# Kernel tuning notes

Hardware: AMD Instinct MI355X
Metric: run time of the kernel (lower is better)

Reference implementation:

```python
import jax, jax.numpy as jnp
import numpy as np

B, N, S, K, R = 4, 8192, 2048, 64, 0.2  # batch, points, centroids, neighbors, ball radius
EPS = 1e-5  # BatchNorm eps


def fps_indices(x, n_samples):
    """Farthest point sampling; returns int32 [B, n_samples] indices."""
    xs = jax.lax.stop_gradient(x)
    Bb, Nn, _ = xs.shape

    def step(carry, _):
        dist, farthest = carry
        centroid = jnp.take_along_axis(xs, farthest[:, None, None], axis=1)  # [B,1,3]
        d = jnp.sum((xs - centroid) ** 2, axis=-1)  # [B,N]
        dist = jnp.minimum(dist, d)
        nxt = jnp.argmax(dist, axis=-1).astype(jnp.int32)
        return (dist, nxt), farthest

    init = (jnp.full((Bb, Nn), 1e10, xs.dtype), jnp.zeros((Bb,), jnp.int32))
    _, idxs = jax.lax.scan(step, init, None, length=n_samples)  # [S,B]
    return jnp.transpose(idxs)  # [B,S]


def ball_query(x, centroids, radius, k):
    """First k point indices within radius of each centroid, -1 padded. int32 [B,S,k]."""
    xs = jax.lax.stop_gradient(x)
    cs = jax.lax.stop_gradient(centroids)
    Nn = xs.shape[1]
    d2 = jnp.sum((cs[:, :, None, :] - xs[:, None, :, :]) ** 2, axis=-1)  # [B,S,N]
    cand = jnp.where(d2 < radius * radius, jnp.arange(Nn, dtype=jnp.int32), Nn)
    neg_topk, _ = jax.lax.top_k(-cand, k)  # k smallest candidate indices
    idx = -neg_topk
    return jnp.where(idx == Nn, -1, idx)


def _forward(x, x_complete, layers, idx_fps, idx_ball):
    centroids = jnp.take_along_axis(x, idx_fps[..., None], axis=1)  # [B,S,3]
    valid = idx_ball >= 0  # [B,S,K]
    sidx = jnp.maximum(idx_ball, 0)
    gather = lambda pts: jax.vmap(lambda p, i: p[i])(pts, sidx)  # [B,S,K,C]
    x_local = gather(x) - centroids[:, :, None, :]  # relative coords
    feats = jnp.concatenate([gather(x_complete), x_local], axis=-1)  # [B,S,K,67]
    h = feats.reshape(B, S * K, -1).transpose(0, 2, 1)  # [B,67,S*K]
    for (W, b, g, bt, m, v) in layers:  # Conv1d(k=1) -> BN(eval) -> ReLU
        h = jnp.einsum('oc,bcn->bon', W, h) + b[None, :, None]
        h = (h - m[None, :, None]) * (g * jax.lax.rsqrt(v + EPS))[None, :, None] + bt[None, :, None]
        h = jax.nn.relu(h)
    h = h.reshape(B, -1, S, K)  # [B,128,S,K]
    h = jnp.where(valid[:, None, :, :], h, -jnp.inf)  # mask invalid neighbors
    pooled = jnp.max(h, axis=3)  # masked max pool over neighborhood
    return centroids, pooled.transpose(0, 2, 1)  # [B,S,3], [B,S,128]


def setup_inputs():
    key = jax.random.key(0)
    ks = jax.random.split(key, 8)
    x = jax.random.uniform(ks[0], (B, N, 3), jnp.float32)
    x_complete = jax.random.normal(ks[1], (B, N, 64), jnp.float32)
    dims = [67, 64, 64, 128]
    inp = {'x': x, 'x_complete': x_complete}
    for i in range(3):
        cin, cout = dims[i], dims[i + 1]
        kk = jax.random.split(ks[2 + i], 6)
        inp[f'W{i+1}'] = jax.random.normal(kk[0], (cout, cin), jnp.float32) * 0.05
        inp[f'b{i+1}'] = jax.random.normal(kk[1], (cout,), jnp.float32) * 0.02
        inp[f'g{i+1}'] = 1.0 + 0.1 * jax.random.normal(kk[2], (cout,), jnp.float32)
        inp[f'bt{i+1}'] = jax.random.normal(kk[3], (cout,), jnp.float32) * 0.02
        inp[f'm{i+1}'] = jax.random.normal(kk[4], (cout,), jnp.float32) * 0.05
        inp[f'v{i+1}'] = jax.random.uniform(kk[5], (cout,), jnp.float32, minval=0.5, maxval=1.5)
    return inp


def reference(x, x_complete, W1, b1, g1, bt1, m1, v1, W2, b2, g2, bt2, m2, v2, W3, b3, g3, bt3, m3, v3):
    idx_fps = fps_indices(x, S)
    cen_sg = jnp.take_along_axis(jax.lax.stop_gradient(x), idx_fps[..., None], axis=1)
    idx_ball = ball_query(x, cen_sg, R, K)
    layers = ((W1, b1, g1, bt1, m1, v1), (W2, b2, g2, bt2, m2, v2), (W3, b3, g3, bt3, m3, v3))
    return _forward(x, x_complete, layers, idx_fps, idx_ball)
```

## Files before the change

kernel.cpp:

```cpp
#include <hip/hip_runtime.h>
#include <math.h>

#define BATCH 4
#define NPTS  8192
#define NSAMP 2048
#define KNBR  64
#define EPSF  1e-5f

typedef float v2f __attribute__((ext_vector_type(2)));

__global__ void prep_kernel(const float* __restrict__ W1, const float* __restrict__ W2,
                            const float* __restrict__ W3,
                            float* __restrict__ W1t, float* __restrict__ W2t,
                            float* __restrict__ W3t) {
    int t = threadIdx.x;
    for (int i = t; i < 64 * 67; i += 256) { int o = i / 67, c = i % 67; W1t[c * 64 + o] = W1[i]; }
    for (int i = t; i < 64 * 64; i += 256) { int o = i >> 6, c = i & 63; W2t[c * 64 + o] = W2[i]; }
    for (int i = t; i < 128 * 64; i += 256) { int o = i >> 6, c = i & 63; W3t[c * 128 + o] = W3[i]; }
}

#define DPP_FMAX(v, ctrl)                                                            \
    do {                                                                             \
        int _t = __builtin_amdgcn_update_dpp(0, __float_as_int(v), ctrl, 0xf, 0xf, true); \
        (v) = fmaxf((v), __int_as_float(_t));                                        \
    } while (0)

__global__ __launch_bounds__(512) void fps_kernel(const float* __restrict__ x,
                                                  float* __restrict__ cen_out) {
#pragma clang fp contract(off)
    const int b = blockIdx.x;
    const int tid = threadIdx.x;
    const int lane = tid & 63;
    const int wid = tid >> 6;
    __shared__ float sx[NPTS], sy[NPTS], sz[NPTS];
    __shared__ __align__(16) float pd[2][8];
    __shared__ int pi[2];
    __shared__ int hist[NSAMP];

    const float* xb = x + (size_t)b * NPTS * 3;
    for (int i = tid; i < NPTS; i += 512) {
        sx[i] = xb[3 * i + 0];
        sy[i] = xb[3 * i + 1];
        sz[i] = xb[3 * i + 2];
    }
    if (tid == 0) { pi[0] = 0x7fffffff; pi[1] = 0x7fffffff; }
    __syncthreads();

    v2f px[8], py[8], pz[8], dist[8];
#pragma unroll
    for (int j = 0; j < 8; j++) {
        int p = tid * 16 + 2 * j;
        px[j] = (v2f){sx[p], sx[p + 1]};
        py[j] = (v2f){sy[p], sy[p + 1]};
        pz[j] = (v2f){sz[p], sz[p + 1]};
        dist[j] = (v2f){1e10f, 1e10f};
    }

    int cur = 0;
    for (int s = 0; s < NSAMP; s++) {
        float cx = sx[cur], cy = sy[cur], cz = sz[cur];
        if (tid == 0) hist[s] = cur;
        const v2f cvx = (v2f){cx, cx}, cvy = (v2f){cy, cy}, cvz = (v2f){cz, cz};
        v2f m = (v2f){-1.0f, -1.0f};
#pragma unroll
        for (int j = 0; j < 8; j++) {
            v2f dx = px[j] - cvx;
            v2f dy = py[j] - cvy;
            v2f dz = pz[j] - cvz;
            v2f d = ((dx * dx) + (dy * dy)) + (dz * dz);
            v2f dm;
            dm.x = fminf(dist[j].x, d.x);
            dm.y = fminf(dist[j].y, d.y);
            dist[j] = dm;
            m.x = fmaxf(m.x, dm.x);
            m.y = fmaxf(m.y, dm.y);
        }
        float bestd = fmaxf(m.x, m.y);
        float w = bestd;
        DPP_FMAX(w, 0x111);
        DPP_FMAX(w, 0x112);
        DPP_FMAX(w, 0x114);
        DPP_FMAX(w, 0x118);
        DPP_FMAX(w, 0x142);
        DPP_FMAX(w, 0x143);
        const int p = s & 1;
        if (lane == 63) pd[p][wid] = w;
        __syncthreads();
        float4 da = *(const float4*)&pd[p][0];
        float4 db = *(const float4*)&pd[p][4];
        float bmax = fmaxf(fmaxf(fmaxf(da.x, da.y), fmaxf(da.z, da.w)),
                           fmaxf(fmaxf(db.x, db.y), fmaxf(db.z, db.w)));
        if (tid == 0) pi[1 - p] = 0x7fffffff;
        int local = 0x7fffffff;
#pragma unroll
        for (int j = 0; j < 8; j++) {
            if (dist[j].x == bmax) local = min(local, tid * 16 + 2 * j);
            if (dist[j].y == bmax) local = min(local, tid * 16 + 2 * j + 1);
        }
        if (local != 0x7fffffff) atomicMin(&pi[p], local);
        __syncthreads();
        cur = pi[p];
    }

    __syncthreads();
    for (int i = tid; i < NSAMP; i += 512) {
        int idx = hist[i];
        float* o = cen_out + ((size_t)b * NSAMP + i) * 3;
        o[0] = sx[idx]; o[1] = sy[idx]; o[2] = sz[idx];
    }
}

__global__ __launch_bounds__(256) void ball_kernel(const float* __restrict__ x,
                                                   const float* __restrict__ cen,
                                                   int* __restrict__ idxb) {
    const int wid = threadIdx.x >> 6, lane = threadIdx.x & 63;
    const int id = blockIdx.x * 4 + wid;
    const int b = id >> 11;
    const float r2 = (float)(0.2 * 0.2);
    const float cx = cen[3 * id], cy = cen[3 * id + 1], cz = cen[3 * id + 2];
    const float* xb = x + (size_t)b * NPTS * 3;

    int count = 0;
    for (int base = 0; base < NPTS && count < KNBR; base += 64) {
        int p = base + lane;
        float pxv = xb[3 * p], pyv = xb[3 * p + 1], pzv = xb[3 * p + 2];
        float dx = __fsub_rn(cx, pxv);
        float dy = __fsub_rn(cy, pyv);
        float dz = __fsub_rn(cz, pzv);
        float d2 = __fadd_rn(__fadd_rn(__fmul_rn(dx, dx), __fmul_rn(dy, dy)), __fmul_rn(dz, dz));
        bool hit = d2 < r2;
        unsigned long long m = __ballot(hit);
        if (hit) {
            int pos = count + __popcll(m & ((1ull << lane) - 1ull));
            if (pos < KNBR) idxb[(size_t)id * KNBR + pos] = p;
        }
        count += (int)__popcll(m);
    }
    for (int pos = count + lane; pos < KNBR; pos += 64)
        idxb[(size_t)id * KNBR + pos] = -1;
}

__global__ __launch_bounds__(256) void mlp_kernel(
    const float* __restrict__ x, const float* __restrict__ xc,
    const float* __restrict__ cen, const int* __restrict__ idxb,
    const float* __restrict__ W1t, const float* __restrict__ b1, const float* __restrict__ g1,
    const float* __restrict__ bt1, const float* __restrict__ m1, const float* __restrict__ v1,
    const float* __restrict__ W2t, const float* __restrict__ b2, const float* __restrict__ g2,
    const float* __restrict__ bt2, const float* __restrict__ m2, const float* __restrict__ v2,
    const float* __restrict__ W3t, const float* __restrict__ b3, const float* __restrict__ g3,
    const float* __restrict__ bt3, const float* __restrict__ m3, const float* __restrict__ v3,
    float* __restrict__ pooled) {
    const int wid = threadIdx.x >> 6, lane = threadIdx.x & 63;
    const int id = blockIdx.x * 4 + wid;
    const int b = id >> 11;
    __shared__ float sred[4][64][33];

    int il = idxb[(size_t)id * KNBR + lane];
    bool valid = il >= 0;
    int ik = valid ? il : 0;

    float cx = cen[3 * id], cy = cen[3 * id + 1], cz = cen[3 * id + 2];
    const float* xp = x + ((size_t)b * NPTS + ik) * 3;
    const float* xcp = xc + ((size_t)b * NPTS + ik) * 64;

    float h1[64];
#pragma unroll
    for (int o = 0; o < 64; o++) h1[o] = 0.f;
#pragma unroll
    for (int c4 = 0; c4 < 16; c4++) {
        float4 t = ((const float4*)xcp)[c4];
        float tv0 = t.x, tv1 = t.y, tv2 = t.z, tv3 = t.w;
#pragma unroll
        for (int o = 0; o < 64; o++) h1[o] = fmaf(W1t[(c4 * 4 + 0) * 64 + o], tv0, h1[o]);
#pragma unroll
        for (int o = 0; o < 64; o++) h1[o] = fmaf(W1t[(c4 * 4 + 1) * 64 + o], tv1, h1[o]);
#pragma unroll
        for (int o = 0; o < 64; o++) h1[o] = fmaf(W1t[(c4 * 4 + 2) * 64 + o], tv2, h1[o]);
#pragma unroll
        for (int o = 0; o < 64; o++) h1[o] = fmaf(W1t[(c4 * 4 + 3) * 64 + o], tv3, h1[o]);
    }
    {
        float xl0 = xp[0] - cx, xl1 = xp[1] - cy, xl2 = xp[2] - cz;
#pragma unroll
        for (int o = 0; o < 64; o++) h1[o] = fmaf(W1t[64 * 64 + o], xl0, h1[o]);
#pragma unroll
        for (int o = 0; o < 64; o++) h1[o] = fmaf(W1t[65 * 64 + o], xl1, h1[o]);
#pragma unroll
        for (int o = 0; o < 64; o++) h1[o] = fmaf(W1t[66 * 64 + o], xl2, h1[o]);
    }
#pragma unroll
    for (int o = 0; o < 64; o++) {
        float sc = g1[o] * rsqrtf(v1[o] + EPSF);
        h1[o] = fmaxf(fmaf(h1[o] + b1[o] - m1[o], sc, bt1[o]), 0.f);
    }

    float h2[64];
#pragma unroll
    for (int o = 0; o < 64; o++) h2[o] = 0.f;
#pragma unroll
    for (int c = 0; c < 64; c++) {
        float hv = h1[c];
#pragma unroll
        for (int o = 0; o < 64; o++) h2[o] = fmaf(W2t[c * 64 + o], hv, h2[o]);
    }
#pragma unroll
    for (int o = 0; o < 64; o++) {
        float sc = g2[o] * rsqrtf(v2[o] + EPSF);
        h2[o] = fmaxf(fmaf(h2[o] + b2[o] - m2[o], sc, bt2[o]), 0.f);
    }

    for (int ch = 0; ch < 4; ch++) {
        float acc[32];
#pragma unroll
        for (int oo = 0; oo < 32; oo++) acc[oo] = 0.f;
#pragma unroll
        for (int c = 0; c < 64; c++) {
            float hv = h2[c];
#pragma unroll
            for (int oo = 0; oo < 32; oo++)
                acc[oo] = fmaf(W3t[c * 128 + ch * 32 + oo], hv, acc[oo]);
        }
#pragma unroll
        for (int oo = 0; oo < 32; oo++) {
            int o = ch * 32 + oo;
            float sc = g3[o] * rsqrtf(v3[o] + EPSF);
            float t = fmaxf(fmaf(acc[oo] + b3[o] - m3[o], sc, bt3[o]), 0.f);
            sred[wid][lane][oo] = valid ? t : -INFINITY;
        }
        __syncthreads();
        {
            int c = lane & 31, half = lane >> 5;
            float mx = -INFINITY;
#pragma unroll
            for (int r = 0; r < 32; r++) mx = fmaxf(mx, sred[wid][half * 32 + r][c]);
            mx = fmaxf(mx, __shfl_xor(mx, 32, 64));
            if (lane < 32) pooled[(size_t)id * 128 + ch * 32 + c] = mx;
        }
        __syncthreads();
    }
}

extern "C" void kernel_launch(void* const* d_in, const int* in_sizes, int n_in,
                              void* d_out, int out_size, void* d_ws, size_t ws_size,
                              hipStream_t stream) {
    const float* x  = (const float*)d_in[0];
    const float* xc = (const float*)d_in[1];
    const float* W1 = (const float*)d_in[2];
    const float* b1 = (const float*)d_in[3];
    const float* g1 = (const float*)d_in[4];
    const float* bt1 = (const float*)d_in[5];
    const float* m1 = (const float*)d_in[6];
    const float* v1 = (const float*)d_in[7];
    const float* W2 = (const float*)d_in[8];
    const float* b2 = (const float*)d_in[9];
    const float* g2 = (const float*)d_in[10];
    const float* bt2 = (const float*)d_in[11];
    const float* m2 = (const float*)d_in[12];
    const float* v2 = (const float*)d_in[13];
    const float* W3 = (const float*)d_in[14];
    const float* b3 = (const float*)d_in[15];
    const float* g3 = (const float*)d_in[16];
    const float* bt3 = (const float*)d_in[17];
    const float* m3 = (const float*)d_in[18];
    const float* v3 = (const float*)d_in[19];

    float* out = (float*)d_out;
    float* cen = out;
    float* pooled = out + (size_t)BATCH * NSAMP * 3;

    int* idxb = (int*)d_ws;
    float* W1t = (float*)((char*)d_ws + (size_t)BATCH * NSAMP * KNBR * 4);
    float* W2t = W1t + 67 * 64;
    float* W3t = W2t + 64 * 64;

    prep_kernel<<<1, 256, 0, stream>>>(W1, W2, W3, W1t, W2t, W3t);
    fps_kernel<<<BATCH, 512, 0, stream>>>(x, cen);
    ball_kernel<<<(BATCH * NSAMP) / 4, 256, 0, stream>>>(x, cen, idxb);
    mlp_kernel<<<(BATCH * NSAMP) / 4, 256, 0, stream>>>(
        x, xc, cen, idxb,
        W1t, b1, g1, bt1, m1, v1,
        W2t, b2, g2, bt2, m2, v2,
        W3t, b3, g3, bt3, m3, v3,
        pooled);
}
```

Measured before the change: 2.418 ms.

## Restructure FPS argmax to one barrier per step with in-wave index selection

The farthest-point-sampling kernel now uses 256 threads, each holding 32 points instead of 16, and builds the per-thread max with a tree reduction. After the DPP max, each wave finds its own argmax through a ballot and readlane. It writes the (value, index) pair to shared memory, so each iteration needs one barrier instead of two plus an atomicMin. This targets the serial per-step synchronisation cost in the 2048-step loop, at the price of more registers per thread and fewer waves to hide latency. Ties across waves still resolve to the lowest index, because the wave comparison uses strict greater-than in wave order.

New measurement: 2.295 ms. -5.1%, faster.

```diff
diff --git a/kernel.cpp b/kernel.cpp
--- a/kernel.cpp
+++ b/kernel.cpp
@@ -25,45 +25,44 @@
         (v) = fmaxf((v), __int_as_float(_t));                                        \
     } while (0)
 
-__global__ __launch_bounds__(512) void fps_kernel(const float* __restrict__ x,
-                                                  float* __restrict__ cen_out) {
+__global__ __launch_bounds__(256, 1) void fps_kernel(const float* __restrict__ x,
+                                                     float* __restrict__ cen_out) {
 #pragma clang fp contract(off)
     const int b = blockIdx.x;
     const int tid = threadIdx.x;
     const int lane = tid & 63;
     const int wid = tid >> 6;
     __shared__ float sx[NPTS], sy[NPTS], sz[NPTS];
-    __shared__ __align__(16) float pd[2][8];
-    __shared__ int pi[2];
+    __shared__ __align__(16) float sd[2][4];
+    __shared__ __align__(16) int   si[2][4];
     __shared__ int hist[NSAMP];
 
     const float* xb = x + (size_t)b * NPTS * 3;
-    for (int i = tid; i < NPTS; i += 512) {
+    for (int i = tid; i < NPTS; i += 256) {
         sx[i] = xb[3 * i + 0];
         sy[i] = xb[3 * i + 1];
         sz[i] = xb[3 * i + 2];
     }
-    if (tid == 0) { pi[0] = 0x7fffffff; pi[1] = 0x7fffffff; }
     __syncthreads();
 
-    v2f px[8], py[8], pz[8], dist[8];
-#pragma unroll
-    for (int j = 0; j < 8; j++) {
-        int p = tid * 16 + 2 * j;
-        px[j] = (v2f){sx[p], sx[p + 1]};
-        py[j] = (v2f){sy[p], sy[p + 1]};
-        pz[j] = (v2f){sz[p], sz[p + 1]};
+    v2f px[16], py[16], pz[16], dist[16];
+    const int base = tid * 32;
+#pragma unroll
+    for (int j = 0; j < 16; j++) {
+        int p = base + 2 * j;
+        px[j] = *(const v2f*)&sx[p];
+        py[j] = *(const v2f*)&sy[p];
+        pz[j] = *(const v2f*)&sz[p];
         dist[j] = (v2f){1e10f, 1e10f};
     }
 
     int cur = 0;
+    float cx = sx[0], cy = sy[0], cz = sz[0];
     for (int s = 0; s < NSAMP; s++) {
-        float cx = sx[cur], cy = sy[cur], cz = sz[cur];
         if (tid == 0) hist[s] = cur;
         const v2f cvx = (v2f){cx, cx}, cvy = (v2f){cy, cy}, cvz = (v2f){cz, cz};
-        v2f m = (v2f){-1.0f, -1.0f};
-#pragma unroll
-        for (int j = 0; j < 8; j++) {
+#pragma unroll
+        for (int j = 0; j < 16; j++) {
             v2f dx = px[j] - cvx;
             v2f dy = py[j] - cvy;
             v2f dz = pz[j] - cvz;
@@ -72,10 +71,18 @@
             dm.x = fminf(dist[j].x, d.x);
             dm.y = fminf(dist[j].y, d.y);
             dist[j] = dm;
-            m.x = fmaxf(m.x, dm.x);
-            m.y = fmaxf(m.y, dm.y);
-        }
-        float bestd = fmaxf(m.x, m.y);
+        }
+        float t[16];
+#pragma unroll
+        for (int j = 0; j < 16; j++) t[j] = fmaxf(dist[j].x, dist[j].y);
+#pragma unroll
+        for (int off = 8; off >= 1; off >>= 1) {
+#pragma unroll
+            for (int j = 0; j < 8; j++)
+                if (j < off) t[j] = fmaxf(t[j], t[j + off]);
+        }
+        float bestd = t[0];
+
         float w = bestd;
         DPP_FMAX(w, 0x111);
         DPP_FMAX(w, 0x112);
@@ -83,27 +90,35 @@
         DPP_FMAX(w, 0x118);
         DPP_FMAX(w, 0x142);
         DPP_FMAX(w, 0x143);
+        const float wmax = __int_as_float(__builtin_amdgcn_readlane(__float_as_int(w), 63));
+
+        unsigned long long mask = __ballot(bestd == wmax);
+        int wl = (int)__builtin_ctzll(mask);
+
+        int lj = 0;
+#pragma unroll
+        for (int j = 15; j >= 0; j--) {
+            if (dist[j].y == wmax) lj = 2 * j + 1;
+            if (dist[j].x == wmax) lj = 2 * j;
+        }
+        int widx = __builtin_amdgcn_readlane(base + lj, wl);
+
         const int p = s & 1;
-        if (lane == 63) pd[p][wid] = w;
+        if (lane == 0) { sd[p][wid] = wmax; si[p][wid] = widx; }
         __syncthreads();
-        float4 da = *(const float4*)&pd[p][0];
-        float4 db = *(const float4*)&pd[p][4];
-        float bmax = fmaxf(fmaxf(fmaxf(da.x, da.y), fmaxf(da.z, da.w)),
-                           fmaxf(fmaxf(db.x, db.y), fmaxf(db.z, db.w)));
-        if (tid == 0) pi[1 - p] = 0x7fffffff;
-        int local = 0x7fffffff;
-#pragma unroll
-        for (int j = 0; j < 8; j++) {
-            if (dist[j].x == bmax) local = min(local, tid * 16 + 2 * j);
-            if (dist[j].y == bmax) local = min(local, tid * 16 + 2 * j + 1);
-        }
-        if (local != 0x7fffffff) atomicMin(&pi[p], local);
-        __syncthreads();
-        cur = pi[p];
+
+        float4 dv = *(const float4*)&sd[p][0];
+        int4   iv = *(const int4*)&si[p][0];
+        float bb = dv.x; int bi = iv.x;
+        if (dv.y > bb) { bb = dv.y; bi = iv.y; }
+        if (dv.z > bb) { bb = dv.z; bi = iv.z; }
+        if (dv.w > bb) { bb = dv.w; bi = iv.w; }
+        cur = bi;
+        cx = sx[cur]; cy = sy[cur]; cz = sz[cur];
     }
 
     __syncthreads();
-    for (int i = tid; i < NSAMP; i += 512) {
+    for (int i = tid; i < NSAMP; i += 256) {
         int idx = hist[i];
         float* o = cen_out + ((size_t)b * NSAMP + i) * 3;
         o[0] = sx[idx]; o[1] = sy[idx]; o[2] = sz[idx];
@@ -274,7 +289,7 @@
     float* W3t = W2t + 64 * 64;
 
     prep_kernel<<<1, 256, 0, stream>>>(W1, W2, W3, W1t, W2t, W3t);
-    fps_kernel<<<BATCH, 512, 0, stream>>>(x, cen);
+    fps_kernel<<<BATCH, 256, 0, stream>>>(x, cen);
     ball_kernel<<<(BATCH * NSAMP) / 4, 256, 0, stream>>>(x, cen, idxb);
     mlp_kernel<<<(BATCH * NSAMP) / 4, 256, 0, stream>>>(
         x, xc, cen, idxb,
```

## Resolve FPS argmax per wave with ballot/readlane, dropping second barrier and atomics

Applied to the files above, without the earlier changes.

Each FPS step now finds the per-wave max and its lowest index in registers using DPP, readlane and ballot. Every wave writes a (value, index) pair to shared memory, and all threads reduce the 8 pairs after a single barrier. This removes the second __syncthreads and the shared atomicMin from every one of the 2048 serial iterations. Points are stored as float4 in LDS so the next centroid comes from one vector load, which adds LDS footprint. Ties across waves go to the lower wave index, and within a wave the first lane wins, which keeps the lowest-index argmax semantics.

Result: faster. 2.345 ms (-3.0%).

```diff
diff --git a/kernel.cpp b/kernel.cpp
--- a/kernel.cpp
+++ b/kernel.cpp
@@ -25,43 +25,42 @@
         (v) = fmaxf((v), __int_as_float(_t));                                        \
     } while (0)
 
-__global__ __launch_bounds__(512) void fps_kernel(const float* __restrict__ x,
-                                                  float* __restrict__ cen_out) {
+__global__ __launch_bounds__(512, 1) void fps_kernel(const float* __restrict__ x,
+                                                     float* __restrict__ cen_out) {
 #pragma clang fp contract(off)
     const int b = blockIdx.x;
     const int tid = threadIdx.x;
     const int lane = tid & 63;
     const int wid = tid >> 6;
-    __shared__ float sx[NPTS], sy[NPTS], sz[NPTS];
-    __shared__ __align__(16) float pd[2][8];
-    __shared__ int pi[2];
+    __shared__ float4 sp[NPTS];
+    __shared__ __align__(32) float sd[2][8];
+    __shared__ __align__(32) int   si[2][8];
     __shared__ int hist[NSAMP];
 
     const float* xb = x + (size_t)b * NPTS * 3;
     for (int i = tid; i < NPTS; i += 512) {
-        sx[i] = xb[3 * i + 0];
-        sy[i] = xb[3 * i + 1];
-        sz[i] = xb[3 * i + 2];
-    }
-    if (tid == 0) { pi[0] = 0x7fffffff; pi[1] = 0x7fffffff; }
+        sp[i] = (float4){xb[3 * i + 0], xb[3 * i + 1], xb[3 * i + 2], 0.f};
+    }
     __syncthreads();
 
     v2f px[8], py[8], pz[8], dist[8];
+    const int base = tid * 16;
 #pragma unroll
     for (int j = 0; j < 8; j++) {
-        int p = tid * 16 + 2 * j;
-        px[j] = (v2f){sx[p], sx[p + 1]};
-        py[j] = (v2f){sy[p], sy[p + 1]};
-        pz[j] = (v2f){sz[p], sz[p + 1]};
+        float4 a = sp[base + 2 * j];
+        float4 c = sp[base + 2 * j + 1];
+        px[j] = (v2f){a.x, c.x};
+        py[j] = (v2f){a.y, c.y};
+        pz[j] = (v2f){a.z, c.z};
         dist[j] = (v2f){1e10f, 1e10f};
     }
 
     int cur = 0;
+    float4 cp = sp[0];
     for (int s = 0; s < NSAMP; s++) {
-        float cx = sx[cur], cy = sy[cur], cz = sz[cur];
         if (tid == 0) hist[s] = cur;
-        const v2f cvx = (v2f){cx, cx}, cvy = (v2f){cy, cy}, cvz = (v2f){cz, cz};
-        v2f m = (v2f){-1.0f, -1.0f};
+        const v2f cvx = (v2f){cp.x, cp.x}, cvy = (v2f){cp.y, cp.y}, cvz = (v2f){cp.z, cp.z};
+        float t[8];
 #pragma unroll
         for (int j = 0; j < 8; j++) {
             v2f dx = px[j] - cvx;
@@ -72,10 +71,12 @@
             dm.x = fminf(dist[j].x, d.x);
             dm.y = fminf(dist[j].y, d.y);
             dist[j] = dm;
-            m.x = fmaxf(m.x, dm.x);
-            m.y = fmaxf(m.y, dm.y);
-        }
-        float bestd = fmaxf(m.x, m.y);
+            t[j] = fmaxf(dm.x, dm.y);
+        }
+        float m01 = fmaxf(t[0], t[1]), m23 = fmaxf(t[2], t[3]);
+        float m45 = fmaxf(t[4], t[5]), m67 = fmaxf(t[6], t[7]);
+        float bestd = fmaxf(fmaxf(m01, m23), fmaxf(m45, m67));
+
         float w = bestd;
         DPP_FMAX(w, 0x111);
         DPP_FMAX(w, 0x112);
@@ -83,30 +84,53 @@
         DPP_FMAX(w, 0x118);
         DPP_FMAX(w, 0x142);
         DPP_FMAX(w, 0x143);
+        const float wmax = __int_as_float(__builtin_amdgcn_readlane(__float_as_int(w), 63));
+
+        unsigned long long mask = __ballot(bestd == wmax);
+        int wl = (int)__builtin_ctzll(mask);
+
+        int c[8];
+#pragma unroll
+        for (int j = 0; j < 8; j++) {
+            int cc = 0x7fffffff;
+            cc = (dist[j].y == wmax) ? (2 * j + 1) : cc;
+            cc = (dist[j].x == wmax) ? (2 * j) : cc;
+            c[j] = cc;
+        }
+        int n01 = min(c[0], c[1]), n23 = min(c[2], c[3]);
+        int n45 = min(c[4], c[5]), n67 = min(c[6], c[7]);
+        int lj = min(min(n01, n23), min(n45, n67));
+        int widx = __builtin_amdgcn_readlane(base + lj, wl);
+
         const int p = s & 1;
-        if (lane == 63) pd[p][wid] = w;
+        if (lane == 0) { sd[p][wid] = wmax; si[p][wid] = widx; }
         __syncthreads();
-        float4 da = *(const float4*)&pd[p][0];
-        float4 db = *(const float4*)&pd[p][4];
-        float bmax = fmaxf(fmaxf(fmaxf(da.x, da.y), fmaxf(da.z, da.w)),
-                           fmaxf(fmaxf(db.x, db.y), fmaxf(db.z, db.w)));
-        if (tid == 0) pi[1 - p] = 0x7fffffff;
-        int local = 0x7fffffff;
-#pragma unroll
-        for (int j = 0; j < 8; j++) {
-            if (dist[j].x == bmax) local = min(local, tid * 16 + 2 * j);
-            if (dist[j].y == bmax) local = min(local, tid * 16 + 2 * j + 1);
-        }
-        if (local != 0x7fffffff) atomicMin(&pi[p], local);
-        __syncthreads();
-        cur = pi[p];
+
+        float4 dva = *(const float4*)&sd[p][0];
+        float4 dvb = *(const float4*)&sd[p][4];
+        int4 iva = *(const int4*)&si[p][0];
+        int4 ivb = *(const int4*)&si[p][4];
+        float v0 = dva.x, v1 = dva.y, v2 = dva.z, v3 = dva.w;
+        float v4 = dvb.x, v5 = dvb.y, v6 = dvb.z, v7 = dvb.w;
+        int i0 = iva.x, i1 = iva.y, i2 = iva.z, i3 = iva.w;
+        int i4 = ivb.x, i5 = ivb.y, i6 = ivb.z, i7 = ivb.w;
+        if (v1 > v0) { v0 = v1; i0 = i1; }
+        if (v3 > v2) { v2 = v3; i2 = i3; }
+        if (v5 > v4) { v4 = v5; i4 = i5; }
+        if (v7 > v6) { v6 = v7; i6 = i7; }
+        if (v2 > v0) { v0 = v2; i0 = i2; }
+        if (v6 > v4) { v4 = v6; i4 = i6; }
+        if (v4 > v0) { v0 = v4; i0 = i4; }
+        cur = i0;
+        cp = sp[cur];
     }
 
     __syncthreads();
     for (int i = tid; i < NSAMP; i += 512) {
         int idx = hist[i];
+        float4 q = sp[idx];
         float* o = cen_out + ((size_t)b * NSAMP + i) * 3;
-        o[0] = sx[idx]; o[1] = sy[idx]; o[2] = sz[idx];
+        o[0] = q.x; o[1] = q.y; o[2] = q.z;
     }
 }
 
```
